# Performance work log

Measured on AMD Instinct MI355X. Metric: run time of the kernel, lower is better.

The kernel has to match this reference:

```python
import jax, jax.numpy as jnp
import numpy as np

KD, KH, KW = 4, 4, 4
SD, SH, SW = 2, 2, 2


def _fold(patches, out_shape):
    """col2im-style overlap-add of 3D volume patches (inverse of extract_volume_patches).

    patches: [B, od, oh, ow, KD*KH*KW*C], TF patch layout is [kd, kh, kw, C] in last dim.
    out_shape: (B, D, H, W, C)
    """
    B, od, oh, ow, _ = patches.shape
    C = out_shape[-1]
    p = patches.reshape(B, od, oh, ow, KD, KH, KW, C)
    out = jnp.zeros(out_shape, patches.dtype)
    # loop over the (small, static) kernel offsets; each offset scatter-adds a
    # strided block -- this is the vectorized scatter-add form of fold.
    for i in range(KD):
        for j in range(KH):
            for l in range(KW):
                out = out.at[:, i:i + SD * od:SD, j:j + SH * oh:SH, l:l + SW * ow:SW, :].add(
                    p[:, :, :, :, i, j, l, :])
    return out


def _overlap_count(D, H, W, od, oh, ow):
    # equals fold(ones) == grad of extract_volume_patches wrt an all-ones cotangent
    cnt = np.zeros((D, H, W), np.float32)
    for i in range(KD):
        for j in range(KH):
            for l in range(KW):
                cnt[i:i + SD * od:SD, j:j + SH * oh:SH, l:l + SW * ow:SW] += 1.0
    return jnp.asarray(cnt)


def setup_inputs() -> dict:
    key = jax.random.key(0)
    k1, k2 = jax.random.split(key)
    B, D, H, W, C = 2, 64, 128, 128, 4
    od = (D - KD) // SD + 1   # 31
    oh = (H - KH) // SH + 1   # 63
    ow = (W - KW) // SW + 1   # 63
    patches = jax.random.normal(k1, (B, od, oh, ow, KD * KH * KW * C), dtype=jnp.float32)
    inputs = jax.random.normal(k2, (B, D, H, W, C), dtype=jnp.float32)
    return {"patches": patches, "inputs": inputs}


def reference(patches, inputs):
    B, D, H, W, C = inputs.shape
    _, od, oh, ow, _ = patches.shape
    acc = _fold(patches, inputs.shape)                # scatter-add of overlapping patches
    cnt = _overlap_count(D, H, W, od, oh, ow)          # per-voxel overlap multiplicity
    return acc / cnt[None, :, :, :, None]
```

## Files before the change

### kernel.cpp

```cpp
#include <hip/hip_runtime.h>


constexpr int Bsz = 2;
constexpr int Dd  = 64;
constexpr int Hh  = 128;
constexpr int Ww  = 128;
constexpr int OD = 31;
constexpr int OH = 63;
constexpr int OW = 63;

__global__ __launch_bounds__(256) void fold_gather_kernel(
    const float4* __restrict__ p, float4* __restrict__ out)
{
    int n = blockIdx.x * 256 + threadIdx.x;
    int w = n & (Ww - 1);
    int h = (n >> 7) & (Hh - 1);
    int d = (n >> 14) & (Dd - 1);
    int b = n >> 20;

    int i0 = d & 1, j0 = h & 1, l0 = w & 1;

    float4 acc = make_float4(0.f, 0.f, 0.f, 0.f);
    int cnt = 0;

    #pragma unroll
    for (int ii = 0; ii < 2; ++ii) {
        int i  = i0 + 2 * ii;
        int zd = (d - i) >> 1;
        if ((unsigned)zd >= (unsigned)OD) continue;
        #pragma unroll
        for (int jj = 0; jj < 2; ++jj) {
            int j  = j0 + 2 * jj;
            int zh = (h - j) >> 1;
            if ((unsigned)zh >= (unsigned)OH) continue;
            #pragma unroll
            for (int ll = 0; ll < 2; ++ll) {
                int l  = l0 + 2 * ll;
                int zw = (w - l) >> 1;
                if ((unsigned)zw >= (unsigned)OW) continue;
                int pidx = ((((b * OD + zd) * OH + zh) * OW + zw) << 6)
                           + (i << 4) + (j << 2) + l;
                float4 v = p[pidx];
                acc.x += v.x; acc.y += v.y; acc.z += v.z; acc.w += v.w;
                ++cnt;
            }
        }
    }

    float inv = 1.0f / (float)cnt;
    acc.x *= inv; acc.y *= inv; acc.z *= inv; acc.w *= inv;
    out[n] = acc;
}

extern "C" void kernel_launch(void* const* d_in, const int* in_sizes, int n_in,
                              void* d_out, int out_size, void* d_ws, size_t ws_size,
                              hipStream_t stream)
{
    const float4* patches = (const float4*)d_in[0];
    float4* out = (float4*)d_out;

    const int total = Bsz * Dd * Hh * Ww;
    fold_gather_kernel<<<total / 256, 256, 0, stream>>>(patches, out);
}
```

Before: 52.66 us.

## Compute even/odd output pairs per thread with adjacent patch loads and nontemporal stores

Each thread now produces two adjacent w outputs, an even and an odd one. For each kernel offset it reads the neighbouring patch entries (l and l+1), which sit next to each other in memory, so every valid patch position costs one pair of contiguous loads. The overlap count is computed in closed form instead of being tallied inside the loop, and the outputs are written with nontemporal stores. In exchange the grid has half as many threads, each carrying more registers and doing more work.

Measured after the change: 53.27 us. Within noise of the previous version (+1.2%).

```diff
diff --git a/kernel.cpp b/kernel.cpp
--- a/kernel.cpp
+++ b/kernel.cpp
@@ -1,64 +1,73 @@
 #include <hip/hip_runtime.h>
 
 
-constexpr int Bsz = 2;
-constexpr int Dd  = 64;
-constexpr int Hh  = 128;
-constexpr int Ww  = 128;
-constexpr int OD = 31;
-constexpr int OH = 63;
-constexpr int OW = 63;
+constexpr int OD = 31, OH = 63, OW = 63;
 
-__global__ __launch_bounds__(256) void fold_gather_kernel(
-    const float4* __restrict__ p, float4* __restrict__ out)
+using f4 = __attribute__((ext_vector_type(4))) float;
+
+__global__ __launch_bounds__(256) void fold_pair_kernel(
+    const f4* __restrict__ p, f4* __restrict__ out)
 {
-    int n = blockIdx.x * 256 + threadIdx.x;
-    int w = n & (Ww - 1);
-    int h = (n >> 7) & (Hh - 1);
-    int d = (n >> 14) & (Dd - 1);
-    int b = n >> 20;
+    int t = blockIdx.x * 256 + threadIdx.x;
+    int q = t & 63;
+    int h = (t >> 6) & 127;
+    int d = (t >> 13) & 63;
+    int b = t >> 19;
 
-    int i0 = d & 1, j0 = h & 1, l0 = w & 1;
+    const int i0 = d & 1, j0 = h & 1;
+    const int zdA = (d - i0) >> 1;
+    const int zhA = (h - j0) >> 1;
 
-    float4 acc = make_float4(0.f, 0.f, 0.f, 0.f);
-    int cnt = 0;
+    const int ci = (zdA <= OD - 1) + (zdA >= 1);
+    const int cj = (zhA <= OH - 1) + (zhA >= 1);
+    const int cl = (q   <= OW - 1) + (q   >= 1);
+    const float inv = 1.0f / (float)(ci * cj * cl);
+
+    const bool qhi = (q <= OW - 1);
+    const bool qlo = (q >= 1);
+
+    f4 ae = (f4)0.0f, ao = (f4)0.0f;
 
     #pragma unroll
     for (int ii = 0; ii < 2; ++ii) {
-        int i  = i0 + 2 * ii;
-        int zd = (d - i) >> 1;
-        if ((unsigned)zd >= (unsigned)OD) continue;
+        const int zd = zdA - ii;
+        if ((unsigned)zd > (unsigned)(OD - 1)) continue;
+        const int i = i0 + 2 * ii;
         #pragma unroll
         for (int jj = 0; jj < 2; ++jj) {
-            int j  = j0 + 2 * jj;
-            int zh = (h - j) >> 1;
-            if ((unsigned)zh >= (unsigned)OH) continue;
-            #pragma unroll
-            for (int ll = 0; ll < 2; ++ll) {
-                int l  = l0 + 2 * ll;
-                int zw = (w - l) >> 1;
-                if ((unsigned)zw >= (unsigned)OW) continue;
-                int pidx = ((((b * OD + zd) * OH + zh) * OW + zw) << 6)
-                           + (i << 4) + (j << 2) + l;
-                float4 v = p[pidx];
-                acc.x += v.x; acc.y += v.y; acc.z += v.z; acc.w += v.w;
-                ++cnt;
+            const int zh = zhA - jj;
+            if ((unsigned)zh > (unsigned)(OH - 1)) continue;
+            const int j = j0 + 2 * jj;
+            const int rowbase = (((b * OD + zd) * OH + zh) * OW) << 6;
+            const int koff = (i << 4) + (j << 2);
+            if (qhi) {
+                const f4* s = p + rowbase + (q << 6) + koff;
+                ae += s[0];
+                ao += s[1];
+            }
+            if (qlo) {
+                const f4* s = p + rowbase + ((q - 1) << 6) + koff + 2;
+                ae += s[0];
+                ao += s[1];
             }
         }
     }
 
-    float inv = 1.0f / (float)cnt;
-    acc.x *= inv; acc.y *= inv; acc.z *= inv; acc.w *= inv;
-    out[n] = acc;
+    ae *= inv;
+    ao *= inv;
+
+    const int n = ((t >> 6) << 7) + (q << 1);
+    __builtin_nontemporal_store(ae, &out[n]);
+    __builtin_nontemporal_store(ao, &out[n + 1]);
 }
 
 extern "C" void kernel_launch(void* const* d_in, const int* in_sizes, int n_in,
                               void* d_out, int out_size, void* d_ws, size_t ws_size,
                               hipStream_t stream)
 {
-    const float4* patches = (const float4*)d_in[0];
-    float4* out = (float4*)d_out;
+    const f4* patches = (const f4*)d_in[0];
+    f4* out = (f4*)d_out;
 
-    const int total = Bsz * Dd * Hh * Ww;
-    fold_gather_kernel<<<total / 256, 256, 0, stream>>>(patches, out);
+    const int total_pairs = 2 * 64 * 128 * 64;
+    fold_pair_kernel<<<total_pairs / 256, 256, 0, stream>>>(patches, out);
 }
```
